# Performance work log

Hardware: AMD Instinct MI355X
Metric: run time of the kernel (lower is better)

The kernel has to match this reference:

```python
import jax, jax.numpy as jnp
import numpy as np
from jax import lax

CONV3_NUM = 5
CONV1_NUM = 1
NEG_SLOPE = 0.2


def _leaky(x):
    return jnp.where(x >= 0, x, NEG_SLOPE * x)


def _per_sample_conv(x, k, b, pad):
    # x: [B,3,H,W], k: [B,3,3,kh,kw] (OIHW per sample), b: [B,3]
    def one(xi, ki, bi):
        y = lax.conv_general_dilated(
            xi[None], ki, (1, 1), ((pad, pad), (pad, pad)),
            dimension_numbers=("NCHW", "OIHW", "NCHW"))[0]
        return y + bi[:, None, None]
    return jax.vmap(one)(x, k, b)


def _conv3x3_block(x, feat):
    B = x.shape[0]
    k = feat[:, :81].reshape(B, 3, 3, 3, 3)
    b = feat[:, 81:84]
    return _leaky(x + _per_sample_conv(x, k, b, 1))


def _conv1x1_block(x, feat):
    B = x.shape[0]
    k = feat[:, :9].reshape(B, 3, 3, 1, 1)
    b = feat[:, 9:12]
    return _leaky(x + _per_sample_conv(x, k, b, 0))


def _att_map(f, h, w, xi):
    # f: [B,20]; h,w: [1,1,H,W]; xi: [B,1,H,W]  -> cubic trivariate polynomial
    c = lambda i: f[:, i][:, None, None, None]
    h2 = h * h; h3 = h2 * h
    w2 = w * w; w3 = w2 * w
    x2 = xi * xi; x3 = x2 * xi
    return (c(0) * h3 + c(1) * h2 * w + c(2) * h2 * xi + c(3) * h2
            + c(4) * h * w2 + c(5) * h * w * xi + c(6) * h * w
            + c(7) * h * x2 + c(8) * h * xi + c(9) * h
            + c(10) * w3 + c(11) * w2 * xi + c(12) * w2
            + c(13) * w * x2 + c(14) * w * xi + c(15) * w
            + c(16) * x3 + c(17) * x2 + c(18) * xi + c(19))


def setup_inputs() -> dict:
    key = jax.random.key(0)
    k1, k2, k3 = jax.random.split(key, 3)
    x = jax.random.normal(k1, (8, 3, 1024, 1024), dtype=jnp.float32)
    thumb_x = jax.random.normal(k2, (8, 3, 256, 256), dtype=jnp.float32)
    # meta() is an external CNN predicting per-sample params; we materialize its
    # output directly (scaled small for numerical stability of the conv stack).
    feature = jax.random.normal(k3, (8, 492), dtype=jnp.float32) * 0.05
    return {"x": x, "thumb_x": thumb_x, "feature": feature}


def reference(x, thumb_x, feature):
    B, _, H, W = x.shape
    residual = x
    for i in range(CONV3_NUM):
        x = _conv3x3_block(x, feature[:, i * 84:(i + 1) * 84])
    off = CONV3_NUM * 84
    for i in range(CONV1_NUM):
        x = _conv1x1_block(x, feature[:, off + i * 12:off + (i + 1) * 12])
    off = off + CONV1_NUM * 12
    x = residual + x
    dt = x.dtype
    h_mat = jnp.broadcast_to((jnp.arange(H, dtype=dt) / H)[None, None, :, None], (1, 1, H, W))
    w_mat = jnp.broadcast_to((jnp.arange(W, dtype=dt) / W)[None, None, None, :], (1, 1, H, W))
    atts = [_att_map(feature[:, off + 20 * c:off + 20 * (c + 1)], h_mat, w_mat, x[:, c:c + 1])
            for c in range(3)]
    att = jnp.concatenate(atts, axis=1)
    x = x * (1 + att)
    # location is None => thumbnail branch is skipped, thumb_x returned as-is
    return (x, thumb_x)
```

## Files before the change

kernel.cpp:

```cpp
#include <hip/hip_runtime.h>
#include <hip/hip_fp16.h>

typedef unsigned int uint;
typedef _Float16 h2 __attribute__((ext_vector_type(2)));


#define ROWS   42
#define W_U    42
#define W_REAL 38
#define CHP_U  (ROWS*W_U)
#define BUF_U  (3*CHP_U)

__device__ __forceinline__ h2   U2H(uint u) { return __builtin_bit_cast(h2, u); }
__device__ __forceinline__ uint H2U(h2 h)   { return __builtin_bit_cast(uint, h); }

__global__ void prep_weights(const float* __restrict__ feat, uint* __restrict__ wtab)
{
    const int b = blockIdx.x;
    const int t = threadIdx.x;
    float w = 0.f;
    bool valid = false;
    if (t < 405) {
        int l = t / 81, r = t % 81;
        int ic = r / 27; r %= 27;
        int ky = r / 9;  r %= 9;
        int oc = r / 3;
        int kx = r % 3;
        w = feat[b * 492 + l * 84 + ((oc * 3 + ic) * 3 + ky) * 3 + kx];
        valid = true;
    } else if (t < 420) {
        int i = t - 405;
        w = feat[b * 492 + (i / 3) * 84 + 81 + (i % 3)];
        valid = true;
    }
    if (valid) {
        _Float16 h = (_Float16)w;
        h2 hh = { h, h };
        wtab[b * 448 + t] = H2U(hh);
    }
}

__global__ __launch_bounds__(512, 6) void fused_net(
    const float* __restrict__ xin,
    const float* __restrict__ thumb,
    const float* __restrict__ feat,
    const uint*  __restrict__ wtab,
    float* __restrict__ out)
{
    const int tid = threadIdx.x;

    if (blockIdx.x == 16) {
        const int part = blockIdx.y + 32 * blockIdx.z;
        const float4* s4 = (const float4*)thumb;
        float4* d4 = (float4*)(out + 25165824ull);
        const int n4 = 1572864 / 4;
        for (int i = part * 512 + tid; i < n4; i += 256 * 512)
            d4[i] = s4[i];
        return;
    }

    const int gx0 = blockIdx.x * 64;
    const int gy0 = blockIdx.y * 32;
    const int b   = blockIdx.z;
    const bool edge = (gx0 == 0) | (gx0 == 960) | (gy0 == 0) | (gy0 == 992);
    const float* wf = feat + b * 492;
    const uint*  wt = wtab + b * 448;

    __shared__ __align__(16) uint lds[2 * BUF_U + 8];
    uint* b0 = lds;
    uint* b1 = lds + BUF_U + 4;

    const float* xb = xin + ((size_t)(b * 3) << 20);
    if (!edge) {
        for (int idx = tid; idx < 3 * ROWS * W_REAL; idx += 512) {
            int ch  = idx / (ROWS * W_REAL);
            int rem = idx - ch * (ROWS * W_REAL);
            int row = rem / W_REAL;
            int u   = rem - row * W_REAL;
            const float2 f = *(const float2*)(xb + ((size_t)ch << 20) +
                                              ((size_t)(gy0 - 5 + row) << 10) +
                                              (gx0 - 6 + 2 * u));
            b0[ch * CHP_U + row * W_U + u] =
                __builtin_bit_cast(uint, __builtin_amdgcn_cvt_pkrtz(f.x, f.y));
        }
    } else {
        for (int idx = tid; idx < 3 * ROWS * W_REAL; idx += 512) {
            int ch  = idx / (ROWS * W_REAL);
            int rem = idx - ch * (ROWS * W_REAL);
            int row = rem / W_REAL;
            int u   = rem - row * W_REAL;
            const int gy = gy0 - 5 + row;
            const int gx = gx0 - 6 + 2 * u;
            float2 f = {0.f, 0.f};
            if ((unsigned)gy < 1024u && (unsigned)gx < 1024u)
                f = *(const float2*)(xb + ((size_t)ch << 20) + ((size_t)gy << 10) + gx);
            b0[ch * CHP_U + row * W_U + u] =
                __builtin_bit_cast(uint, __builtin_amdgcn_cvt_pkrtz(f.x, f.y));
        }
    }
    __syncthreads();

    const int er  = tid >> 5;
    const int uc  = tid & 31;
    const int ub0 = (5 + er) * W_U + 3 + uc;
    const int ub1 = ub0 + 16 * W_U;
    uint resu[2][3];
    #pragma unroll
    for (int ch = 0; ch < 3; ++ch) {
        resu[0][ch] = b0[ch * CHP_U + ub0];
        resu[1][ch] = b0[ch * CHP_U + ub1];
    }

    const int cr = tid / 18;
    const int cc = tid - cr * 18;
    const int y0 = 1 + 2 * cr;
    const int x0 = 2 + 4 * cc;
    uint mA[2] = {~0u, ~0u}, mB[2] = {~0u, ~0u};
    if (edge) {
        const int gyA = gy0 - 5 + y0;
        const int gxA = gx0 - 6 + x0;
        const uint mA0 = ((((unsigned)gxA       < 1024u) ? 0x0000ffffu : 0u) |
                          (((unsigned)(gxA + 1) < 1024u) ? 0xffff0000u : 0u));
        const uint mB0 = ((((unsigned)(gxA + 2) < 1024u) ? 0x0000ffffu : 0u) |
                          (((unsigned)(gxA + 3) < 1024u) ? 0xffff0000u : 0u));
        #pragma unroll
        for (int j = 0; j < 2; ++j) {
            const uint mr = ((unsigned)(gyA + j) < 1024u) ? ~0u : 0u;
            mA[j] = mA0 & mr;
            mB[j] = mB0 & mr;
        }
    }

    const h2 c02 = { (_Float16)0.2f, (_Float16)0.2f };

    #pragma unroll
    for (int l = 0; l < 5; ++l) {
        const uint* sb = (l & 1) ? b1 : b0;
        uint*       db = (l & 1) ? b0 : b1;
        if (tid < 360) {
            const uint* tb = sb + (y0 - 1) * W_U + 2 * cc;
            uint*       ob = db + y0 * W_U + 1 + 2 * cc;
            h2 accA[2][3], accB[2][3];
            #pragma unroll
            for (int oc = 0; oc < 3; ++oc) {
                const h2 bi = U2H(wt[405 + l * 3 + oc]);
                accA[0][oc] = bi; accA[1][oc] = bi;
                accB[0][oc] = bi; accB[1][oc] = bi;
            }
            #pragma unroll
            for (int ic = 0; ic < 3; ++ic) {
                #pragma unroll
                for (int t = 0; t < 4; ++t) {
                    const uint2 P = *(const uint2*)(tb + ic * CHP_U + t * W_U);
                    const uint2 Q = *(const uint2*)(tb + ic * CHP_U + t * W_U + 2);
                    const uint u0 = P.x, u1 = P.y, u2 = Q.x, u3 = Q.y;
                    const h2 X01 = U2H((u0 >> 16) | (u1 << 16));
                    const h2 C1  = U2H(u1);
                    const h2 X12 = U2H((u1 >> 16) | (u2 << 16));
                    const h2 C2  = U2H(u2);
                    const h2 X23 = U2H((u2 >> 16) | (u3 << 16));
                    #pragma unroll
                    for (int j = 0; j < 2; ++j) {
                        const int ky = t - j;
                        if (0 <= ky && ky <= 2) {
                            const int wb = l * 81 + (ic * 3 + ky) * 9;
                            #pragma unroll
                            for (int oc = 0; oc < 3; ++oc) {
                                const h2 w0 = U2H(wt[wb + oc * 3 + 0]);
                                const h2 w1 = U2H(wt[wb + oc * 3 + 1]);
                                const h2 w2 = U2H(wt[wb + oc * 3 + 2]);
                                accA[j][oc] = __builtin_elementwise_fma(w0, X01, accA[j][oc]);
                                accA[j][oc] = __builtin_elementwise_fma(w1, C1,  accA[j][oc]);
                                accA[j][oc] = __builtin_elementwise_fma(w2, X12, accA[j][oc]);
                                accB[j][oc] = __builtin_elementwise_fma(w0, X12, accB[j][oc]);
                                accB[j][oc] = __builtin_elementwise_fma(w1, C2,  accB[j][oc]);
                                accB[j][oc] = __builtin_elementwise_fma(w2, X23, accB[j][oc]);
                            }
                        }
                    }
                    if (t == 1) { accA[0][ic] = accA[0][ic] + C1; accB[0][ic] = accB[0][ic] + C2; }
                    if (t == 2) { accA[1][ic] = accA[1][ic] + C1; accB[1][ic] = accB[1][ic] + C2; }
                }
            }
            #pragma unroll
            for (int j = 0; j < 2; ++j) {
                #pragma unroll
                for (int oc = 0; oc < 3; ++oc) {
                    h2 vA = accA[j][oc]; vA = __builtin_elementwise_max(vA, c02 * vA);
                    h2 vB = accB[j][oc]; vB = __builtin_elementwise_max(vB, c02 * vB);
                    ob[oc * CHP_U + j * W_U]     = H2U(vA) & mA[j];
                    ob[oc * CHP_U + j * W_U + 1] = H2U(vB) & mB[j];
                }
            }
        }
        __syncthreads();
    }

    float* outb = out + ((size_t)(b * 3) << 20);
    #pragma unroll
    for (int rr = 0; rr < 2; ++rr) {
        const int ub = rr ? ub1 : ub0;
        const int gy = gy0 + er + 16 * rr;
        float x5f[3][2], resf[3][2];
        #pragma unroll
        for (int ch = 0; ch < 3; ++ch) {
            h2 hr = U2H(resu[rr][ch]);
            resf[ch][0] = (float)hr.x; resf[ch][1] = (float)hr.y;
            h2 hx = U2H(b1[ch * CHP_U + ub]);
            x5f[ch][0] = (float)hx.x; x5f[ch][1] = (float)hx.y;
        }
        const float h1 = (float)gy * (1.0f / 1024.0f);
        const float h2v = h1 * h1, h3 = h2v * h1;
        float tmp[3][2];
        #pragma unroll
        for (int j = 0; j < 2; ++j) {
            const float wc = (float)(gx0 + 2 * uc + j) * (1.0f / 1024.0f);
            const float w2 = wc * wc, w3 = w2 * wc;
            const float hw = h1 * wc, h2w = h2v * wc, hw2 = h1 * w2;
            #pragma unroll
            for (int oc = 0; oc < 3; ++oc) {
                float s = x5f[oc][j] + wf[429 + oc]
                        + wf[420 + oc * 3 + 0] * x5f[0][j]
                        + wf[420 + oc * 3 + 1] * x5f[1][j]
                        + wf[420 + oc * 3 + 2] * x5f[2][j];
                s = s >= 0.f ? s : 0.2f * s;
                const float xf = resf[oc][j] + s;
                const float x1 = xf, x2 = x1 * x1, x3 = x2 * x1;
                const float* cf = wf + 432 + oc * 20;
                float att =
                    cf[0] * h3 + cf[1] * h2w + cf[2] * h2v * x1 + cf[3] * h2v +
                    cf[4] * hw2 + cf[5] * hw * x1 + cf[6] * hw + cf[7] * h1 * x2 +
                    cf[8] * h1 * x1 + cf[9] * h1 + cf[10] * w3 + cf[11] * w2 * x1 +
                    cf[12] * w2 + cf[13] * wc * x2 + cf[14] * wc * x1 + cf[15] * wc +
                    cf[16] * x3 + cf[17] * x2 + cf[18] * x1 + cf[19];
                tmp[oc][j] = xf * (1.f + att);
            }
        }
        #pragma unroll
        for (int oc = 0; oc < 3; ++oc) {
            float2 v = {tmp[oc][0], tmp[oc][1]};
            *(float2*)&outb[((size_t)oc << 20) + ((size_t)gy << 10) + (gx0 + 2 * uc)] = v;
        }
    }
}

extern "C" void kernel_launch(void* const* d_in, const int* in_sizes, int n_in,
                              void* d_out, int out_size, void* d_ws, size_t ws_size,
                              hipStream_t stream) {
    const float* x     = (const float*)d_in[0];
    const float* thumb = (const float*)d_in[1];
    const float* feat  = (const float*)d_in[2];
    float* out = (float*)d_out;
    uint* wtab = (uint*)d_ws;

    prep_weights<<<dim3(8), 448, 0, stream>>>(feat, wtab);
    dim3 grid(17, 32, 8);
    fused_net<<<grid, 512, 0, stream>>>(x, thumb, feat, wtab, out);
}
```

Before: 302.4 us.

## Shrink LDS row pitch, raise occupancy, unroll tile load, skip masks on interior tiles

Reduces the LDS row pitch from 42 to 40 uints, shrinking the shared buffer so more blocks fit per CU, and raises the launch-bounds minimum blocks from 6 to 8. Replaces the div/mod-indexed tile load loop with a fully unrolled 10-iteration loop that updates row, column and channel incrementally. Interior tiles skip the zero-padding mask AND when writing intermediate activations. The tighter register budget risks spills, and the new pitch may change LDS bank-conflict patterns.

```diff
diff --git a/kernel.cpp b/kernel.cpp
--- a/kernel.cpp
+++ b/kernel.cpp
@@ -6,7 +6,7 @@
 
 
 #define ROWS   42
-#define W_U    42
+#define W_U    40
 #define W_REAL 38
 #define CHP_U  (ROWS*W_U)
 #define BUF_U  (3*CHP_U)
@@ -40,7 +40,7 @@
     }
 }
 
-__global__ __launch_bounds__(512, 6) void fused_net(
+__global__ __launch_bounds__(512, 8) void fused_net(
     const float* __restrict__ xin,
     const float* __restrict__ thumb,
     const float* __restrict__ feat,
@@ -71,31 +71,41 @@
     uint* b1 = lds + BUF_U + 4;
 
     const float* xb = xin + ((size_t)(b * 3) << 20);
-    if (!edge) {
-        for (int idx = tid; idx < 3 * ROWS * W_REAL; idx += 512) {
-            int ch  = idx / (ROWS * W_REAL);
-            int rem = idx - ch * (ROWS * W_REAL);
-            int row = rem / W_REAL;
-            int u   = rem - row * W_REAL;
-            const float2 f = *(const float2*)(xb + ((size_t)ch << 20) +
-                                              ((size_t)(gy0 - 5 + row) << 10) +
-                                              (gx0 - 6 + 2 * u));
-            b0[ch * CHP_U + row * W_U + u] =
-                __builtin_bit_cast(uint, __builtin_amdgcn_cvt_pkrtz(f.x, f.y));
-        }
-    } else {
-        for (int idx = tid; idx < 3 * ROWS * W_REAL; idx += 512) {
-            int ch  = idx / (ROWS * W_REAL);
-            int rem = idx - ch * (ROWS * W_REAL);
-            int row = rem / W_REAL;
-            int u   = rem - row * W_REAL;
-            const int gy = gy0 - 5 + row;
-            const int gx = gx0 - 6 + 2 * u;
-            float2 f = {0.f, 0.f};
-            if ((unsigned)gy < 1024u && (unsigned)gx < 1024u)
-                f = *(const float2*)(xb + ((size_t)ch << 20) + ((size_t)gy << 10) + gx);
-            b0[ch * CHP_U + row * W_U + u] =
-                __builtin_bit_cast(uint, __builtin_amdgcn_cvt_pkrtz(f.x, f.y));
+    {
+        int srow = tid / 38;
+        int su   = tid - srow * 38;
+        int sch  = 0;
+        if (!edge) {
+            #pragma unroll
+            for (int it = 0; it < 10; ++it) {
+                if (it < 9 || tid < 180) {
+                    const float2 f = *(const float2*)(xb + ((size_t)sch << 20) +
+                                                      ((size_t)(gy0 - 5 + srow) << 10) +
+                                                      (gx0 - 6 + 2 * su));
+                    b0[sch * CHP_U + srow * W_U + su] =
+                        __builtin_bit_cast(uint, __builtin_amdgcn_cvt_pkrtz(f.x, f.y));
+                }
+                su += 18; srow += 13;
+                if (su >= 38)   { su -= 38; srow += 1; }
+                if (srow >= 42) { srow -= 42; sch += 1; }
+            }
+        } else {
+            #pragma unroll
+            for (int it = 0; it < 10; ++it) {
+                if (it < 9 || tid < 180) {
+                    const int gy = gy0 - 5 + srow;
+                    const int gx = gx0 - 6 + 2 * su;
+                    float2 f = {0.f, 0.f};
+                    if ((unsigned)gy < 1024u && (unsigned)gx < 1024u)
+                        f = *(const float2*)(xb + ((size_t)sch << 20) +
+                                             ((size_t)gy << 10) + gx);
+                    b0[sch * CHP_U + srow * W_U + su] =
+                        __builtin_bit_cast(uint, __builtin_amdgcn_cvt_pkrtz(f.x, f.y));
+                }
+                su += 18; srow += 13;
+                if (su >= 38)   { su -= 38; srow += 1; }
+                if (srow >= 42) { srow -= 42; sch += 1; }
+            }
         }
     }
     __syncthreads();
@@ -182,14 +192,27 @@
                     if (t == 2) { accA[1][ic] = accA[1][ic] + C1; accB[1][ic] = accB[1][ic] + C2; }
                 }
             }
-            #pragma unroll
-            for (int j = 0; j < 2; ++j) {
+            if (!edge) {
                 #pragma unroll
-                for (int oc = 0; oc < 3; ++oc) {
-                    h2 vA = accA[j][oc]; vA = __builtin_elementwise_max(vA, c02 * vA);
-                    h2 vB = accB[j][oc]; vB = __builtin_elementwise_max(vB, c02 * vB);
-                    ob[oc * CHP_U + j * W_U]     = H2U(vA) & mA[j];
-                    ob[oc * CHP_U + j * W_U + 1] = H2U(vB) & mB[j];
+                for (int j = 0; j < 2; ++j) {
+                    #pragma unroll
+                    for (int oc = 0; oc < 3; ++oc) {
+                        h2 vA = accA[j][oc]; vA = __builtin_elementwise_max(vA, c02 * vA);
+                        h2 vB = accB[j][oc]; vB = __builtin_elementwise_max(vB, c02 * vB);
+                        ob[oc * CHP_U + j * W_U]     = H2U(vA);
+                        ob[oc * CHP_U + j * W_U + 1] = H2U(vB);
+                    }
+                }
+            } else {
+                #pragma unroll
+                for (int j = 0; j < 2; ++j) {
+                    #pragma unroll
+                    for (int oc = 0; oc < 3; ++oc) {
+                        h2 vA = accA[j][oc]; vA = __builtin_elementwise_max(vA, c02 * vA);
+                        h2 vB = accB[j][oc]; vB = __builtin_elementwise_max(vB, c02 * vB);
+                        ob[oc * CHP_U + j * W_U]     = H2U(vA) & mA[j];
+                        ob[oc * CHP_U + j * W_U + 1] = H2U(vB) & mB[j];
+                    }
                 }
             }
         }
```

Result: faster. 288.4 us (-4.6%).
